# Optimization experiments

Hardware: AMD Instinct MI355X
Metric: run time of the kernel (lower is better)

The kernel has to match this reference:

```python
import jax, jax.numpy as jnp
import numpy as np

RE_PER_PRB = 12  # resource elements (subcarriers) per PRB in 5G NR


def _forward(y, h_hat_ls, dmrs_ofdm_pos, dmrs_subcarrier_pos):
    S = y.shape[2]  # num_ofdm_symbols (y used for its shape only)
    # [B, num_pilots, T, R] -> [B, R, T, num_pilots]
    h = jnp.transpose(h_hat_ls, (0, 3, 2, 1))
    B, R, T, P = h.shape
    # FOCC removal: average adjacent pilot pairs, duplicate back (sum/2, repeat 2)
    h = h.reshape(B, R, T, P // 2, 2).sum(axis=-1, keepdims=True) * 0.5
    h = jnp.broadcast_to(h, (B, R, T, P // 2, 2)).reshape(B, R, T, P)

    npd = dmrs_subcarrier_pos.shape[1]   # pilots per DMRS symbol per PRB
    nds = dmrs_ofdm_pos.shape[-1]        # number of DMRS OFDM symbols
    nprb = P // (npd * nds)              # number of PRBs
    RE = RE_PER_PRB

    # --- nearest-pilot indices + positional encodings, per tx (as in torch code,
    # torch.meshgrid default indexing='ij') ---
    re_pos = jnp.stack(
        jnp.meshgrid(jnp.arange(RE), jnp.arange(S), indexing='ij'), axis=-1
    ).reshape(-1, 1, 2)  # [RE*S, 1, 2]

    def per_tx(sc_pos, of_pos):
        pil = jnp.stack(jnp.meshgrid(sc_pos, of_pos, indexing='ij'), axis=-1).reshape(1, -1, 2)
        diff = jnp.abs(re_pos - pil)                  # [RE*S, npd*nds, 2] Manhattan components
        nn = jnp.argmin(diff.sum(-1), axis=1).reshape(S, RE)
        pe = diff.min(axis=1).reshape(S, RE, 2).transpose(1, 0, 2).astype(jnp.float32)  # [RE, S, 2]
        norm = lambda x: (x - x.mean()) / (x.std(ddof=1) + 1e-8)  # torch .std() is unbiased
        # channel order swapped exactly as in the torch code: [time-dist, freq-dist]
        return nn, jnp.stack([norm(pe[..., 1]), norm(pe[..., 0])], axis=-1)

    nn_idx, pe = jax.vmap(per_tx)(dmrs_subcarrier_pos, dmrs_ofdm_pos)  # [T,S,RE], [T,RE,S,2]
    pe = jnp.tile(pe, (1, nprb, 1, 1))  # [T, nprb*RE, S, 2]

    # --- group pilots per PRB ---
    # pilot layout in h_hat_ls: (dmrs_symbol, prb, subcarrier); per-PRB pilot index
    # = subcarrier*nds + symbol to match the meshgrid('ij') flattening above
    hp = h.reshape(B, R, T, nds, nprb, npd).transpose(0, 1, 2, 4, 5, 3)
    hp = hp.reshape(B, R, T, nprb, npd * nds)  # [B,R,T,nprb,pilots_per_prb]

    # --- nearest-neighbor gather onto the full resource grid ---
    gather_tx = lambda hp_t, nn_t: hp_t[..., nn_t]  # [B,R,nprb,Np] , [S,RE] -> [B,R,nprb,S,RE]
    gathered = jax.vmap(gather_tx, in_axes=(2, 0), out_axes=2)(hp, nn_idx)  # [B,R,T,nprb,S,RE]

    # -> [B, T, num_subcarriers, S, R]
    h_full = gathered.transpose(0, 2, 3, 5, 4, 1).reshape(B, T, nprb * RE, S, R)
    return h_full, pe


def setup_inputs() -> dict:
    key = jax.random.key(0)
    k1, k2 = jax.random.split(key)
    B, R, T, S = 16, 16, 4, 14
    nprb, npd, nds = 273, 6, 2
    P = nds * nprb * npd  # 3276 pilots
    y = jax.random.normal(k1, (B, R, S, nprb * RE_PER_PRB), dtype=jnp.float32)
    h_hat_ls = jax.random.normal(k2, (B, P, T, R), dtype=jnp.float32)
    dmrs_ofdm_pos = jnp.broadcast_to(jnp.array([2, 11], dtype=jnp.int32), (T, nds))
    dmrs_subcarrier_pos = jnp.broadcast_to(jnp.arange(0, 12, 2, dtype=jnp.int32), (T, npd))
    return {"y": y, "h_hat_ls": h_hat_ls, "dmrs_ofdm_pos": dmrs_ofdm_pos,
            "dmrs_subcarrier_pos": dmrs_subcarrier_pos}


def reference(y, h_hat_ls, dmrs_ofdm_pos, dmrs_subcarrier_pos):
    return _forward(y, h_hat_ls, dmrs_ofdm_pos, dmrs_subcarrier_pos)
```

## Files before the change

### kernel.cpp

```cpp
#include <hip/hip_runtime.h>

#define B_   16
#define R_   16
#define T_   4
#define S_   14
#define NPRB 273
#define NPD  6
#define NDS  2
#define RE_  12
#define P_   (NDS*NPRB*NPD)
#define NSC  (NPRB*RE_)
#define F_   (RE_*S_)

#define NH   (B_*T_*NSC*S_*R_)
#define NPE  (T_*NSC*S_*2)
#define NH4  (NH/4)
#define NPE4 (NPE/4)
#define NTOT4 (NH4+NPE4)

typedef float vf4 __attribute__((ext_vector_type(4)));

__global__ __launch_bounds__(256) void prep_tables(
    const int* __restrict__ ofdm_pos,
    const int* __restrict__ sc_pos,
    int* __restrict__ qtab,
    float* __restrict__ pe_base)
{
    __shared__ float dt_sh[T_*F_];
    __shared__ float df_sh[T_*F_];
    __shared__ float stats[T_][4];
    __shared__ int   sc_sh[T_*NPD];
    __shared__ int   of_sh[T_*NDS];

    const int tid = threadIdx.x;
    if (tid < T_*NPD) sc_sh[tid] = sc_pos[tid];
    if (tid < T_*NDS) of_sh[tid] = ofdm_pos[tid];
    __syncthreads();

    for (int e = tid; e < T_*F_; e += 256) {
        const int t = e / F_, f = e % F_;
        const int re = f / S_, s = f % S_;
        int best = 1 << 30, bestj = 0;
        int dfmin = 1 << 30, dtmin = 1 << 30;
        #pragma unroll
        for (int sci = 0; sci < NPD; ++sci) {
            const int dsc = abs(re - sc_sh[t*NPD + sci]);
            if (dsc < dfmin) dfmin = dsc;
            #pragma unroll
            for (int ofi = 0; ofi < NDS; ++ofi) {
                const int dof = abs(s - of_sh[t*NDS + ofi]);
                const int d = dsc + dof;
                if (d < best) { best = d; bestj = sci*NDS + ofi; }
            }
        }
        #pragma unroll
        for (int ofi = 0; ofi < NDS; ++ofi) {
            const int dof = abs(s - of_sh[t*NDS + ofi]);
            if (dof < dtmin) dtmin = dof;
        }
        const int sc = bestj / NDS, ds = bestj % NDS;
        qtab[e] = ds*(NPRB*NPD) + (sc & ~1);
        dt_sh[e] = (float)dtmin;
        df_sh[e] = (float)dfmin;
    }
    __syncthreads();

    const int w = tid >> 6, lane = tid & 63;
    {
        float st = 0.f, sf = 0.f;
        for (int i = lane; i < F_; i += 64) { st += dt_sh[w*F_+i]; sf += df_sh[w*F_+i]; }
        #pragma unroll
        for (int off = 32; off >= 1; off >>= 1) {
            st += __shfl_xor(st, off);
            sf += __shfl_xor(sf, off);
        }
        const float mt = st / (float)F_, mf = sf / (float)F_;
        float vt = 0.f, vf = 0.f;
        for (int i = lane; i < F_; i += 64) {
            const float a = dt_sh[w*F_+i] - mt; vt += a*a;
            const float b = df_sh[w*F_+i] - mf; vf += b*b;
        }
        #pragma unroll
        for (int off = 32; off >= 1; off >>= 1) {
            vt += __shfl_xor(vt, off);
            vf += __shfl_xor(vf, off);
        }
        if (lane == 0) {
            const float stdt = sqrtf(vt / (float)(F_-1));
            const float stdf = sqrtf(vf / (float)(F_-1));
            stats[w][0] = mt; stats[w][1] = 1.0f/(stdt + 1e-8f);
            stats[w][2] = mf; stats[w][3] = 1.0f/(stdf + 1e-8f);
        }
    }
    __syncthreads();

    for (int e = tid; e < T_*F_; e += 256) {
        const int t = e / F_;
        pe_base[e*2 + 0] = (dt_sh[e] - stats[t][0]) * stats[t][1];
        pe_base[e*2 + 1] = (df_sh[e] - stats[t][2]) * stats[t][3];
    }
}

__global__ __launch_bounds__(256) void gather_kernel(
    const float* __restrict__ hls,
    const int* __restrict__ qtab,
    const float* __restrict__ pe_base,
    float* __restrict__ out)
{
    __shared__ int   qtab_s[T_*F_];
    __shared__ float pe_s[T_*F_*2];
    const int tid = threadIdx.x;
    for (int i = tid; i < T_*F_; i += 256)   qtab_s[i] = qtab[i];
    for (int i = tid; i < T_*F_*2; i += 256) pe_s[i]   = pe_base[i];
    __syncthreads();

    const int idx = blockIdx.x * blockDim.x + tid;
    if (idx >= NTOT4) return;
    if (idx < NH4) {
        const int r4 = idx & 3;
        int u = idx >> 2;
        const int s = u % S_;  u /= S_;
        const int k = u % NSC; u /= NSC;
        const int t = u & (T_-1);
        const int b = u >> 2;
        const int prb = k / RE_;
        const int re  = k - prb*RE_;
        const int f  = s*RE_ + re;
        const int p0 = qtab_s[t*F_ + f] + prb*NPD;
        const vf4* src = (const vf4*)hls + ((b*P_ + p0)*T_ + t)*(R_/4) + r4;
        const vf4 a = src[0];
        const vf4 c = src[T_*(R_/4)];
        const vf4 o = 0.5f*(a + c);
        __builtin_nontemporal_store(o, (vf4*)out + idx);
    } else {
        const int g0 = (idx - NH4) * 4;
        vf4 o;
        #pragma unroll
        for (int u2 = 0; u2 < 4; ++u2) {
            const int g  = g0 + u2;
            const int c  = g & 1;
            const int g1 = g >> 1;
            const int s  = g1 % S_;
            const int g2 = g1 / S_;
            const int i  = g2 % NSC;
            const int t  = g2 / NSC;
            const int re = i % RE_;
            o[u2] = pe_s[(t*F_ + s*RE_ + re)*2 + c];
        }
        __builtin_nontemporal_store(o, (vf4*)(out + NH) + (idx - NH4));
    }
}

extern "C" void kernel_launch(void* const* d_in, const int* in_sizes, int n_in,
                              void* d_out, int out_size, void* d_ws, size_t ws_size,
                              hipStream_t stream) {
    const float* hls  = (const float*)d_in[1];
    const int*   ofdm = (const int*)d_in[2];
    const int*   scp  = (const int*)d_in[3];
    float* out = (float*)d_out;

    int*   qtab    = (int*)d_ws;
    float* pe_base = (float*)((char*)d_ws + T_*F_*sizeof(int));

    hipLaunchKernelGGL(prep_tables, dim3(1), dim3(256), 0, stream,
                       ofdm, scp, qtab, pe_base);

    const int blocks = (NTOT4 + 255) / 256;
    hipLaunchKernelGGL(gather_kernel, dim3(blocks), dim3(256), 0, stream,
                       hls, qtab, pe_base, out);
}
```

Baseline: 266.0 us.

## Give each thread a full R row and drop LDS table staging

Each thread now handles all 16 receive antennas for one (b,t,k,s) point, with four vf4 loads from each of two adjacent pilots and four vf4 stores. This cuts index arithmetic and the table lookup to one per 16 outputs. The LDS copy of the qtab and pe tables, along with its barrier, is removed, so lookups read global memory through the cache. Nontemporal stores become regular stores. The trade-off is that each thread writes a contiguous 64 bytes, so accesses across a wave become strided per instruction instead of fully coalesced.

Result: no change. 265.3 us (-0.3%).

```diff
diff --git a/kernel.cpp b/kernel.cpp
--- a/kernel.cpp
+++ b/kernel.cpp
@@ -12,11 +12,12 @@
 #define NSC  (NPRB*RE_)
 #define F_   (RE_*S_)
 
-#define NH   (B_*T_*NSC*S_*R_)
-#define NPE  (T_*NSC*S_*2)
-#define NH4  (NH/4)
-#define NPE4 (NPE/4)
-#define NTOT4 (NH4+NPE4)
+#define NH    (B_*T_*NSC*S_*R_)
+#define NPE   (T_*NSC*S_*2)
+#define NPE4  (NPE/4)
+#define NTH   (B_*T_*NSC*S_)
+#define HBLOCKS (NTH/256)
+#define PEBLOCKS ((NPE4+255)/256)
 
 typedef float vf4 __attribute__((ext_vector_type(4)));
 
@@ -107,18 +108,11 @@
     const float* __restrict__ pe_base,
     float* __restrict__ out)
 {
-    __shared__ int   qtab_s[T_*F_];
-    __shared__ float pe_s[T_*F_*2];
     const int tid = threadIdx.x;
-    for (int i = tid; i < T_*F_; i += 256)   qtab_s[i] = qtab[i];
-    for (int i = tid; i < T_*F_*2; i += 256) pe_s[i]   = pe_base[i];
-    __syncthreads();
-
-    const int idx = blockIdx.x * blockDim.x + tid;
-    if (idx >= NTOT4) return;
-    if (idx < NH4) {
-        const int r4 = idx & 3;
-        int u = idx >> 2;
+    const int bid = blockIdx.x;
+    if (bid < HBLOCKS) {
+        const int idx = bid*256 + tid;
+        int u = idx;
         const int s = u % S_;  u /= S_;
         const int k = u % NSC; u /= NSC;
         const int t = u & (T_-1);
@@ -126,28 +120,34 @@
         const int prb = k / RE_;
         const int re  = k - prb*RE_;
         const int f  = s*RE_ + re;
-        const int p0 = qtab_s[t*F_ + f] + prb*NPD;
-        const vf4* src = (const vf4*)hls + ((b*P_ + p0)*T_ + t)*(R_/4) + r4;
-        const vf4 a = src[0];
-        const vf4 c = src[T_*(R_/4)];
-        const vf4 o = 0.5f*(a + c);
-        __builtin_nontemporal_store(o, (vf4*)out + idx);
+        const int p0 = qtab[t*F_ + f] + prb*NPD;
+        const vf4* src = (const vf4*)hls + ((b*P_ + p0)*T_ + t)*(R_/4);
+        vf4 a[4], c[4];
+        #pragma unroll
+        for (int j = 0; j < 4; ++j) a[j] = src[j];
+        #pragma unroll
+        for (int j = 0; j < 4; ++j) c[j] = src[T_*(R_/4) + j];
+        vf4* dst = (vf4*)out + idx*4;
+        #pragma unroll
+        for (int j = 0; j < 4; ++j) dst[j] = 0.5f*(a[j] + c[j]);
     } else {
-        const int g0 = (idx - NH4) * 4;
+        const int idx4 = (bid - HBLOCKS)*256 + tid;
+        if (idx4 >= NPE4) return;
+        const int g0 = idx4 * 4;
         vf4 o;
         #pragma unroll
         for (int u2 = 0; u2 < 4; ++u2) {
             const int g  = g0 + u2;
-            const int c  = g & 1;
+            const int ch = g & 1;
             const int g1 = g >> 1;
             const int s  = g1 % S_;
             const int g2 = g1 / S_;
             const int i  = g2 % NSC;
             const int t  = g2 / NSC;
             const int re = i % RE_;
-            o[u2] = pe_s[(t*F_ + s*RE_ + re)*2 + c];
+            o[u2] = pe_base[(t*F_ + s*RE_ + re)*2 + ch];
         }
-        __builtin_nontemporal_store(o, (vf4*)(out + NH) + (idx - NH4));
+        ((vf4*)(out + NH))[idx4] = o;
     }
 }
 
@@ -165,7 +165,6 @@
     hipLaunchKernelGGL(prep_tables, dim3(1), dim3(256), 0, stream,
                        ofdm, scp, qtab, pe_base);
 
-    const int blocks = (NTOT4 + 255) / 256;
-    hipLaunchKernelGGL(gather_kernel, dim3(blocks), dim3(256), 0, stream,
-                       hls, qtab, pe_base, out);
+    hipLaunchKernelGGL(gather_kernel, dim3(HBLOCKS + PEBLOCKS), dim3(256), 0,
+                       stream, hls, qtab, pe_base, out);
 }
```
